# Performance work log

Hardware: AMD Instinct MI355X
Metric: run time of the kernel (lower is better)

The kernel has to match this reference:

```python
import jax, jax.numpy as jnp
import numpy as np

N_NODES = 100000
N_EDGES = 1600000
D = 64


def setup_inputs() -> dict:
    key = jax.random.key(0)
    ks = jax.random.split(key, 9)
    x = jax.random.normal(ks[0], (N_NODES, D), dtype=jnp.float32)
    src = jax.random.randint(ks[1], (N_EDGES,), 0, N_NODES, dtype=jnp.int64)
    dst = jax.random.randint(ks[2], (N_EDGES,), 0, N_NODES, dtype=jnp.int64)
    s = 1.0 / np.sqrt(D)
    W_self1 = jax.random.normal(ks[3], (D, D), dtype=jnp.float32) * s
    W_neigh1 = jax.random.normal(ks[4], (D, D), dtype=jnp.float32) * s
    b1 = jnp.zeros((D,), dtype=jnp.float32)
    W_self2 = jax.random.normal(ks[5], (D, D), dtype=jnp.float32) * s
    W_neigh2 = jax.random.normal(ks[6], (D, D), dtype=jnp.float32) * s
    b2 = jnp.zeros((D,), dtype=jnp.float32)
    return {"x": x, "src": src, "dst": dst,
            "W_self1": W_self1, "W_neigh1": W_neigh1, "b1": b1,
            "W_self2": W_self2, "W_neigh2": W_neigh2, "b2": b2}


def _sage_layer(h, src, dst, W_self, W_neigh, b, n_nodes):
    # gather source-node features along edges: [E, d]
    msg = h[src]
    # sum messages into destination nodes, then normalize by in-degree (mean agg)
    agg = jax.ops.segment_sum(msg, dst, num_segments=n_nodes)
    deg = jax.ops.segment_sum(jnp.ones((src.shape[0], 1), h.dtype), dst,
                              num_segments=n_nodes)
    h_neigh = agg / jnp.maximum(deg, 1.0)
    # DGL SAGEConv (mean): fc_self(h) + fc_neigh(h_neigh) + bias
    return h @ W_self + h_neigh @ W_neigh + b


def reference(x, src, dst, W_self1, W_neigh1, b1, W_self2, W_neigh2, b2):
    n = x.shape[0]
    h = _sage_layer(x, src, dst, W_self1, W_neigh1, b1, n)
    # note: source module's forward applies no activation between layers
    h = _sage_layer(h, src, dst, W_self2, W_neigh2, b2, n)
    return h
```

## Files before the change

### kernel.cpp

```cpp
#include <hip/hip_runtime.h>
#include <hip/hip_bf16.h>


#define D 64
#define CAP 64
#define BNODES 256
#define BCAP 4736
#define MAXNB 512
#define WT_STRIDE 144

typedef __bf16 bf16x8 __attribute__((ext_vector_type(8)));
typedef float  f32x4  __attribute__((ext_vector_type(4)));

__device__ __forceinline__ unsigned pack2(float a, float b) {
    __hip_bfloat162 t = __float22bfloat162_rn(make_float2(a, b));
    return *(unsigned*)&t;
}
__device__ __forceinline__ unsigned short f2b(float f) {
    __hip_bfloat16 b = __float2bfloat16(f);
    return *(unsigned short*)&b;
}


__global__ void __launch_bounds__(256)
prep_kernel(const float4* __restrict__ x, uint4* __restrict__ xb4,
            unsigned* __restrict__ xsent, unsigned* __restrict__ h1sent,
            int* __restrict__ esent,
            const int* __restrict__ src, const int* __restrict__ dst,
            int* __restrict__ gcur, int* __restrict__ gbucket,
            int E, int NB, int n8, int bin_blocks, int N) {
    const int bid = blockIdx.x;
    const int t   = threadIdx.x;

    if (bid < bin_blocks) {
        __shared__ int hist[MAXNB];
        for (int i = t; i < NB; i += 256) hist[i] = 0;
        __syncthreads();

        const int e4_total = E >> 2;
        const int base4    = bid * 1024;

        int4 sv[4], dv[4];
        bool have[4];
        #pragma unroll
        for (int k = 0; k < 4; ++k) {
            int i4 = base4 + t + k * 256;
            have[k] = i4 < e4_total;
            if (have[k]) {
                sv[k] = ((const int4*)src)[i4];
                dv[k] = ((const int4*)dst)[i4];
            }
        }

        #pragma unroll
        for (int k = 0; k < 4; ++k) if (have[k]) {
            atomicAdd(&hist[dv[k].x >> 8], 1);
            atomicAdd(&hist[dv[k].y >> 8], 1);
            atomicAdd(&hist[dv[k].z >> 8], 1);
            atomicAdd(&hist[dv[k].w >> 8], 1);
        }

        int  tail_s = 0, tail_d = 0;
        bool have_tail = false;
        if (bid == 0) {
            int e = (e4_total << 2) + t;
            if (e < E) {
                tail_s = src[e]; tail_d = dst[e]; have_tail = true;
                atomicAdd(&hist[tail_d >> 8], 1);
            }
        }
        __syncthreads();

        for (int i = t; i < NB; i += 256) {
            int c = hist[i];
            hist[i] = (c > 0) ? atomicAdd(&gcur[i], c) : 0;
        }
        __syncthreads();

        #pragma unroll
        for (int k = 0; k < 4; ++k) if (have[k]) {
            int4 s = sv[k], d = dv[k];
            int b, p;
            b = d.x >> 8; p = atomicAdd(&hist[b], 1); if (p < BCAP) gbucket[b * BCAP + p] = ((d.x & 255) << 17) | s.x;
            b = d.y >> 8; p = atomicAdd(&hist[b], 1); if (p < BCAP) gbucket[b * BCAP + p] = ((d.y & 255) << 17) | s.y;
            b = d.z >> 8; p = atomicAdd(&hist[b], 1); if (p < BCAP) gbucket[b * BCAP + p] = ((d.z & 255) << 17) | s.z;
            b = d.w >> 8; p = atomicAdd(&hist[b], 1); if (p < BCAP) gbucket[b * BCAP + p] = ((d.w & 255) << 17) | s.w;
        }
        if (have_tail) {
            int b = tail_d >> 8, p = atomicAdd(&hist[b], 1);
            if (p < BCAP) gbucket[b * BCAP + p] = ((tail_d & 255) << 17) | tail_s;
        }
        return;
    }

    const int cb = bid - bin_blocks;
    const int i  = cb * 256 + t;
    if (i < n8) {
        float4 a = x[2 * i], b = x[2 * i + 1];
        uint4 o;
        o.x = pack2(a.x, a.y);
        o.y = pack2(a.z, a.w);
        o.z = pack2(b.x, b.y);
        o.w = pack2(b.z, b.w);
        xb4[i] = o;
    }
    if (cb == 0) {
        if (t < 32)              xsent[t] = 0u;
        else if (t < 64)         h1sent[t - 32] = 0u;
        else if (t < 64 + CAP)   esent[t - 64] = N;
    }
}


__global__ void __launch_bounds__(256)
ellify_kernel(const int* __restrict__ gcur, const int* __restrict__ gbucket,
              int* __restrict__ cnt, int* __restrict__ edge_idx, int N) {
    __shared__ int scnt[BNODES];
    scnt[threadIdx.x] = 0;
    __syncthreads();

    const int b     = blockIdx.x;
    const int ne    = min(gcur[b], BCAP);
    const int node0 = b << 8;

    for (int e = threadIdx.x; e < ne; e += 256) {
        int p   = gbucket[b * BCAP + e];
        int s   = p & 0x1FFFF;
        int ld  = p >> 17;
        int pos = atomicAdd(&scnt[ld], 1);
        if (pos < CAP) edge_idx[(size_t)(node0 + ld) * CAP + pos] = s;
    }
    __syncthreads();

    int node = node0 + threadIdx.x;
    if (node < N) {
        int raw = scnt[threadIdx.x];
        cnt[node] = raw;
        int c  = min(raw, CAP);
        int c8 = (c + 7) & ~7;
        for (int p = c; p < c8; ++p)
            edge_idx[(size_t)node * CAP + p] = N;
    }
}


__device__ __forceinline__ void acc8(float& a0, float& a1, float& a2, float& a3,
                                     float& a4, float& a5, float& a6, float& a7,
                                     uint4 u) {
    a0 += __uint_as_float(u.x << 16);
    a1 += __uint_as_float(u.x & 0xffff0000u);
    a2 += __uint_as_float(u.y << 16);
    a3 += __uint_as_float(u.y & 0xffff0000u);
    a4 += __uint_as_float(u.z << 16);
    a5 += __uint_as_float(u.z & 0xffff0000u);
    a6 += __uint_as_float(u.w << 16);
    a7 += __uint_as_float(u.w & 0xffff0000u);
}

__device__ __forceinline__ bf16x8 asbf(uint4 u) {
    union { uint4 a; bf16x8 v; } c; c.a = u; return c.v;
}

__global__ void __launch_bounds__(256, 3)
fused_kernel(const unsigned short* __restrict__ h,
             const int* __restrict__ cnt,
             const int* __restrict__ edge_idx,
             const float* __restrict__ Wself,
             const float* __restrict__ Wneigh,
             const float* __restrict__ bias,
             float* __restrict__ out_f32,
             unsigned short* __restrict__ out_bf16, int N) {
    __shared__ __align__(16) unsigned short wt[64 * WT_STRIDE];

    {
        const int t    = threadIdx.x;
        const int krow = t >> 1;
        const int c0   = (t & 1) * 32;
        const float* Wrow = (krow < 64) ? (Wself + krow * 64)
                                        : (Wneigh + (krow - 64) * 64);
        for (int i = 0; i < 32; i += 4) {
            float4 w = *(const float4*)(Wrow + c0 + i);
            const int n0 = c0 + i;
            wt[(n0 + 0) * WT_STRIDE + krow] = f2b(w.x);
            wt[(n0 + 1) * WT_STRIDE + krow] = f2b(w.y);
            wt[(n0 + 2) * WT_STRIDE + krow] = f2b(w.z);
            wt[(n0 + 3) * WT_STRIDE + krow] = f2b(w.w);
        }
    }
    __syncthreads();

    const int lane = threadIdx.x & 63;
    const int q    = lane & 7;
    const int g    = lane >> 3;
    const int col  = lane & 15;
    const int quad = lane >> 4;
    const int wave = blockIdx.x * (blockDim.x >> 6) + (threadIdx.x >> 6);
    const int n_waves = gridDim.x * (blockDim.x >> 6);

    float bv[4];
    #pragma unroll
    for (int nt = 0; nt < 4; ++nt) bv[nt] = bias[nt * 16 + col];

    const uint4* __restrict__ h4 = (const uint4*)h;
    const int SENT = N * CAP;

    const int tiles = (N + 15) >> 4;
    for (int t = wave; t < tiles; t += n_waves) {
        const int nodeA = t * 16 + g;
        const int nodeB = nodeA + 8;
        const int cA = (nodeA < N) ? min(cnt[nodeA], CAP) : 0;
        const int cB = (nodeB < N) ? min(cnt[nodeB], CAP) : 0;
        const int c8A = (cA + 7) & ~7;
        const int c8B = (cB + 7) & ~7;
        const int startA = ((nodeA < N) ? nodeA : 0) * CAP;
        const int startB = ((nodeB < N) ? nodeB : 0) * CAP;
        const int cmax = max(c8A, c8B);
        const int b0   = g << 3;

        float a0 = 0.f, a1 = 0.f, a2 = 0.f, a3 = 0.f;
        float a4 = 0.f, a5 = 0.f, a6 = 0.f, a7 = 0.f;
        float b0f = 0.f, b1f = 0.f, b2f = 0.f, b3f = 0.f;
        float b4f = 0.f, b5f = 0.f, b6f = 0.f, b7f = 0.f;

        int srA = edge_idx[((0 < c8A) ? startA : SENT) + q];
        int srB = edge_idx[((0 < c8B) ? startB : SENT) + q];

        for (int j = 0; j < cmax; j += 8) {
            const int jn = j + 8;
            const int srA_n = edge_idx[((jn < c8A) ? startA + jn : SENT) + q];
            const int srB_n = edge_idx[((jn < c8B) ? startB + jn : SENT) + q];

            const int sA0 = __shfl(srA, b0 + 0, 64);
            const int sA1 = __shfl(srA, b0 + 1, 64);
            const int sA2 = __shfl(srA, b0 + 2, 64);
            const int sA3 = __shfl(srA, b0 + 3, 64);
            const int sA4 = __shfl(srA, b0 + 4, 64);
            const int sA5 = __shfl(srA, b0 + 5, 64);
            const int sA6 = __shfl(srA, b0 + 6, 64);
            const int sA7 = __shfl(srA, b0 + 7, 64);
            const int sB0 = __shfl(srB, b0 + 0, 64);
            const int sB1 = __shfl(srB, b0 + 1, 64);
            const int sB2 = __shfl(srB, b0 + 2, 64);
            const int sB3 = __shfl(srB, b0 + 3, 64);
            const int sB4 = __shfl(srB, b0 + 4, 64);
            const int sB5 = __shfl(srB, b0 + 5, 64);
            const int sB6 = __shfl(srB, b0 + 6, 64);
            const int sB7 = __shfl(srB, b0 + 7, 64);

            uint4 uA0 = h4[(size_t)sA0 * 8 + q];
            uint4 uA1 = h4[(size_t)sA1 * 8 + q];
            uint4 uA2 = h4[(size_t)sA2 * 8 + q];
            uint4 uA3 = h4[(size_t)sA3 * 8 + q];
            uint4 uA4 = h4[(size_t)sA4 * 8 + q];
            uint4 uA5 = h4[(size_t)sA5 * 8 + q];
            uint4 uA6 = h4[(size_t)sA6 * 8 + q];
            uint4 uA7 = h4[(size_t)sA7 * 8 + q];
            uint4 uB0 = h4[(size_t)sB0 * 8 + q];
            uint4 uB1 = h4[(size_t)sB1 * 8 + q];
            uint4 uB2 = h4[(size_t)sB2 * 8 + q];
            uint4 uB3 = h4[(size_t)sB3 * 8 + q];
            uint4 uB4 = h4[(size_t)sB4 * 8 + q];
            uint4 uB5 = h4[(size_t)sB5 * 8 + q];
            uint4 uB6 = h4[(size_t)sB6 * 8 + q];
            uint4 uB7 = h4[(size_t)sB7 * 8 + q];

            __builtin_amdgcn_sched_barrier(0);

            acc8(a0, a1, a2, a3, a4, a5, a6, a7, uA0);
            acc8(a0, a1, a2, a3, a4, a5, a6, a7, uA1);
            acc8(a0, a1, a2, a3, a4, a5, a6, a7, uA2);
            acc8(a0, a1, a2, a3, a4, a5, a6, a7, uA3);
            acc8(a0, a1, a2, a3, a4, a5, a6, a7, uA4);
            acc8(a0, a1, a2, a3, a4, a5, a6, a7, uA5);
            acc8(a0, a1, a2, a3, a4, a5, a6, a7, uA6);
            acc8(a0, a1, a2, a3, a4, a5, a6, a7, uA7);
            acc8(b0f, b1f, b2f, b3f, b4f, b5f, b6f, b7f, uB0);
            acc8(b0f, b1f, b2f, b3f, b4f, b5f, b6f, b7f, uB1);
            acc8(b0f, b1f, b2f, b3f, b4f, b5f, b6f, b7f, uB2);
            acc8(b0f, b1f, b2f, b3f, b4f, b5f, b6f, b7f, uB3);
            acc8(b0f, b1f, b2f, b3f, b4f, b5f, b6f, b7f, uB4);
            acc8(b0f, b1f, b2f, b3f, b4f, b5f, b6f, b7f, uB5);
            acc8(b0f, b1f, b2f, b3f, b4f, b5f, b6f, b7f, uB6);
            acc8(b0f, b1f, b2f, b3f, b4f, b5f, b6f, b7f, uB7);

            srA = srA_n;
            srB = srB_n;
        }

        const float invA = 1.0f / fmaxf((float)cA, 1.0f);
        const float invB = 1.0f / fmaxf((float)cB, 1.0f);
        uint4 P0, P1;
        P0.x = pack2(a0 * invA, a1 * invA);
        P0.y = pack2(a2 * invA, a3 * invA);
        P0.z = pack2(a4 * invA, a5 * invA);
        P0.w = pack2(a6 * invA, a7 * invA);
        P1.x = pack2(b0f * invB, b1f * invB);
        P1.y = pack2(b2f * invB, b3f * invB);
        P1.z = pack2(b4f * invB, b5f * invB);
        P1.w = pack2(b6f * invB, b7f * invB);

        int row = t * 16 + col;
        if (row >= N) row = N - 1;
        uint4 A0u = h4[(size_t)row * 8 + quad];
        uint4 A1u = h4[(size_t)row * 8 + 4 + quad];

        const int srcA2 = ((lane & 7) << 3) + quad;
        const int srcA3 = srcA2 + 4;
        const bool hi   = (lane & 8) != 0;
        uint4 A2u, A3u;
        {
            unsigned l0 = __shfl(P0.x, srcA2, 64), h0 = __shfl(P1.x, srcA2, 64);
            unsigned l1 = __shfl(P0.y, srcA2, 64), h1 = __shfl(P1.y, srcA2, 64);
            unsigned l2 = __shfl(P0.z, srcA2, 64), h2 = __shfl(P1.z, srcA2, 64);
            unsigned l3 = __shfl(P0.w, srcA2, 64), h3 = __shfl(P1.w, srcA2, 64);
            A2u.x = hi ? h0 : l0;  A2u.y = hi ? h1 : l1;
            A2u.z = hi ? h2 : l2;  A2u.w = hi ? h3 : l3;
        }
        {
            unsigned l0 = __shfl(P0.x, srcA3, 64), h0 = __shfl(P1.x, srcA3, 64);
            unsigned l1 = __shfl(P0.y, srcA3, 64), h1 = __shfl(P1.y, srcA3, 64);
            unsigned l2 = __shfl(P0.z, srcA3, 64), h2 = __shfl(P1.z, srcA3, 64);
            unsigned l3 = __shfl(P0.w, srcA3, 64), h3 = __shfl(P1.w, srcA3, 64);
            A3u.x = hi ? h0 : l0;  A3u.y = hi ? h1 : l1;
            A3u.z = hi ? h2 : l2;  A3u.w = hi ? h3 : l3;
        }

        bf16x8 A0 = asbf(A0u), A1 = asbf(A1u);
        bf16x8 A2 = asbf(A2u), A3 = asbf(A3u);

        __builtin_amdgcn_sched_barrier(0);
        int ob = 0;
        asm volatile("" : "+v"(ob));
        bf16x8 Bf[4][4];
        #pragma unroll
        for (int nt = 0; nt < 4; ++nt) {
            const int n = nt * 16 + col;
            #pragma unroll
            for (int kk = 0; kk < 4; ++kk) {
                const int kcat0 = ((kk >= 2) ? 64 : 0) + (kk & 1) * 32 + quad * 8;
                const char* p = (const char*)wt + n * (WT_STRIDE * 2) + kcat0 * 2 + ob;
                Bf[nt][kk] = *(const bf16x8*)p;
            }
        }

        #pragma unroll
        for (int nt = 0; nt < 4; ++nt) {
            f32x4 acc = {bv[nt], bv[nt], bv[nt], bv[nt]};
            acc = __builtin_amdgcn_mfma_f32_16x16x32_bf16(A0, Bf[nt][0], acc, 0, 0, 0);
            acc = __builtin_amdgcn_mfma_f32_16x16x32_bf16(A1, Bf[nt][1], acc, 0, 0, 0);
            acc = __builtin_amdgcn_mfma_f32_16x16x32_bf16(A2, Bf[nt][2], acc, 0, 0, 0);
            acc = __builtin_amdgcn_mfma_f32_16x16x32_bf16(A3, Bf[nt][3], acc, 0, 0, 0);
            if (out_f32) {
                #pragma unroll
                for (int r = 0; r < 4; ++r) {
                    const int orow = t * 16 + quad * 4 + r;
                    if (orow < N) out_f32[(size_t)orow * D + nt * 16 + col] = acc[r];
                }
            } else {
                #pragma unroll
                for (int r = 0; r < 4; ++r) {
                    const int orow = t * 16 + quad * 4 + r;
                    if (orow < N) out_bf16[(size_t)orow * D + nt * 16 + col] = f2b(acc[r]);
                }
            }
        }
    }
}


extern "C" void kernel_launch(void* const* d_in, const int* in_sizes, int n_in,
                              void* d_out, int out_size, void* d_ws, size_t ws_size,
                              hipStream_t stream) {
    const float* x   = (const float*)d_in[0];
    const int*   src = (const int*)d_in[1];
    const int*   dst = (const int*)d_in[2];
    const float* Ws1 = (const float*)d_in[3];
    const float* Wn1 = (const float*)d_in[4];
    const float* b1  = (const float*)d_in[5];
    const float* Ws2 = (const float*)d_in[6];
    const float* Wn2 = (const float*)d_in[7];
    const float* b2  = (const float*)d_in[8];

    const int N = in_sizes[0] / D;
    const int E = in_sizes[1];

    float* out = (float*)d_out;

    const int NB = (N + BNODES - 1) / BNODES;

    int* gcur      = (int*)d_ws;
    int* cnt       = gcur + 512;
    int* edge_idx  = cnt + N;
    unsigned short* xb   = (unsigned short*)(edge_idx + (size_t)(N + 1) * CAP);
    unsigned short* h1b  = xb + (size_t)(N + 1) * D;
    int* gbucket   = (int*)(h1b + (size_t)(N + 1) * D);

    const int n8         = N * D / 8;
    const int cvt_blocks = (n8 + 255) / 256;
    const int e4_total   = E >> 2;
    const int bin_blocks = (e4_total + 1023) / 1024 > 0 ? (e4_total + 1023) / 1024 : 1;

    hipMemsetAsync(gcur, 0, 512 * sizeof(int), stream);

    prep_kernel<<<bin_blocks + cvt_blocks, 256, 0, stream>>>(
        (const float4*)x, (uint4*)xb,
        (unsigned*)(xb + (size_t)N * D), (unsigned*)(h1b + (size_t)N * D),
        edge_idx + (size_t)N * CAP,
        src, dst, gcur, gbucket, E, NB, n8, bin_blocks, N);

    ellify_kernel<<<NB, 256, 0, stream>>>(gcur, gbucket, cnt, edge_idx, N);

    const int tiles   = (N + 15) / 16;
    const int fblocks = (tiles + 3) / 4;

    fused_kernel<<<fblocks, 256, 0, stream>>>(xb, cnt, edge_idx, Ws1, Wn1, b1,
                                              nullptr, h1b, N);
    fused_kernel<<<fblocks, 256, 0, stream>>>(h1b, cnt, edge_idx, Ws2, Wn2, b2,
                                              out, nullptr, N);
}
```

Before: 204.0 us.

## Use persistent grid with software-prefetched next-tile degree and edge indices

The fused layer kernel now launches a fixed 768-block persistent grid instead of one wave per tile. Each wave loops over tiles and prefetches the next tile's degree counts and first edge indices while working on the current one. The self-feature row loads are hoisted ahead of the gather loop so their latency overlaps with aggregation. The cost is more live registers and a hardcoded grid size that may not match occupancy on this GPU.

```diff
diff --git a/kernel.cpp b/kernel.cpp
--- a/kernel.cpp
+++ b/kernel.cpp
@@ -197,6 +197,10 @@
     const int wave = blockIdx.x * (blockDim.x >> 6) + (threadIdx.x >> 6);
     const int n_waves = gridDim.x * (blockDim.x >> 6);
 
+    const int tiles = (N + 15) >> 4;
+    int t = wave;
+    if (t >= tiles) return;
+
     float bv[4];
     #pragma unroll
     for (int nt = 0; nt < 4; ++nt) bv[nt] = bias[nt * 16 + col];
@@ -204,26 +208,50 @@
     const uint4* __restrict__ h4 = (const uint4*)h;
     const int SENT = N * CAP;
 
-    const int tiles = (N + 15) >> 4;
-    for (int t = wave; t < tiles; t += n_waves) {
-        const int nodeA = t * 16 + g;
-        const int nodeB = nodeA + 8;
-        const int cA = (nodeA < N) ? min(cnt[nodeA], CAP) : 0;
-        const int cB = (nodeB < N) ? min(cnt[nodeB], CAP) : 0;
-        const int c8A = (cA + 7) & ~7;
-        const int c8B = (cB + 7) & ~7;
+    int pcA, pcB, psrA, psrB;
+    {
+        const int nodeA = t * 16 + g, nodeB = nodeA + 8;
+        const int aA = (nodeA < N) ? nodeA : 0;
+        const int aB = (nodeB < N) ? nodeB : 0;
+        const int lA = cnt[aA], lB = cnt[aB];
+        pcA  = (nodeA < N) ? lA : 0;
+        pcB  = (nodeB < N) ? lB : 0;
+        psrA = edge_idx[aA * CAP + q];
+        psrB = edge_idx[aB * CAP + q];
+    }
+
+    for (; t < tiles; t += n_waves) {
+        const int cA  = min(pcA, CAP), cB = min(pcB, CAP);
+        const int c8A = (cA + 7) & ~7, c8B = (cB + 7) & ~7;
+        const int nodeA  = t * 16 + g;
         const int startA = ((nodeA < N) ? nodeA : 0) * CAP;
-        const int startB = ((nodeB < N) ? nodeB : 0) * CAP;
+        const int startB = ((nodeA + 8 < N) ? nodeA + 8 : 0) * CAP;
         const int cmax = max(c8A, c8B);
         const int b0   = g << 3;
+        int srA = psrA, srB = psrB;
+
+        {
+            const int tn = t + n_waves;
+            const int tc = (tn < tiles) ? tn : t;
+            const int nA = tc * 16 + g, nB = nA + 8;
+            const int aA = (nA < N) ? nA : 0;
+            const int aB = (nB < N) ? nB : 0;
+            const int lA = cnt[aA], lB = cnt[aB];
+            pcA  = (nA < N) ? lA : 0;
+            pcB  = (nB < N) ? lB : 0;
+            psrA = edge_idx[aA * CAP + q];
+            psrB = edge_idx[aB * CAP + q];
+        }
+
+        int row = t * 16 + col;
+        if (row >= N) row = N - 1;
+        uint4 A0u = h4[(size_t)row * 8 + quad];
+        uint4 A1u = h4[(size_t)row * 8 + 4 + quad];
 
         float a0 = 0.f, a1 = 0.f, a2 = 0.f, a3 = 0.f;
         float a4 = 0.f, a5 = 0.f, a6 = 0.f, a7 = 0.f;
         float b0f = 0.f, b1f = 0.f, b2f = 0.f, b3f = 0.f;
         float b4f = 0.f, b5f = 0.f, b6f = 0.f, b7f = 0.f;
-
-        int srA = edge_idx[((0 < c8A) ? startA : SENT) + q];
-        int srB = edge_idx[((0 < c8B) ? startB : SENT) + q];
 
         for (int j = 0; j < cmax; j += 8) {
             const int jn = j + 8;
@@ -287,8 +315,8 @@
             srB = srB_n;
         }
 
-        const float invA = 1.0f / fmaxf((float)cA, 1.0f);
-        const float invB = 1.0f / fmaxf((float)cB, 1.0f);
+        const float invA = (cA > 0) ? 1.0f / (float)cA : 0.0f;
+        const float invB = (cB > 0) ? 1.0f / (float)cB : 0.0f;
         uint4 P0, P1;
         P0.x = pack2(a0 * invA, a1 * invA);
         P0.y = pack2(a2 * invA, a3 * invA);
@@ -298,11 +326,6 @@
         P1.y = pack2(b2f * invB, b3f * invB);
         P1.z = pack2(b4f * invB, b5f * invB);
         P1.w = pack2(b6f * invB, b7f * invB);
-
-        int row = t * 16 + col;
-        if (row >= N) row = N - 1;
-        uint4 A0u = h4[(size_t)row * 8 + quad];
-        uint4 A1u = h4[(size_t)row * 8 + 4 + quad];
 
         const int srcA2 = ((lane & 7) << 3) + quad;
         const int srcA3 = srcA2 + 4;
@@ -410,8 +433,7 @@
 
     ellify_kernel<<<NB, 256, 0, stream>>>(gcur, gbucket, cnt, edge_idx, N);
 
-    const int tiles   = (N + 15) / 16;
-    const int fblocks = (tiles + 3) / 4;
+    const int fblocks = 768;
 
     fused_kernel<<<fblocks, 256, 0, stream>>>(xb, cnt, edge_idx, Ws1, Wn1, b1,
                                               nullptr, h1b, N);
```

New measurement: 197.7 us. -3.1%, faster.
